# Kernel optimization log

Hardware: AMD Instinct MI355X
Metric: run time of the kernel (lower is better)

The kernel has to match this reference:

```python
import jax, jax.numpy as jnp
import numpy as np

N_MID = 100000
D = 64
B = 64
S = 256
K = 10
BIG_NEG = -2.0**32 + 1.0


def _din(q, facts, mask, W1, b1, W2, b2, W3, b3):
    # q broadcastable to facts shape; facts [..., T, D]; mask [..., T]
    qb = jnp.broadcast_to(q, facts.shape)
    x = jnp.concatenate([qb, facts, qb - facts, qb * facts], axis=-1)  # [..., T, 4D]
    h = jax.nn.sigmoid(x @ W1 + b1)
    h = jax.nn.sigmoid(h @ W2 + b2)
    s = (h @ W3 + b3)[..., 0]  # [..., T]
    s = jnp.where(mask == 1.0, s, BIG_NEG)
    a = jax.nn.softmax(s, axis=-1)
    return jnp.einsum('...t,...td->...d', a, facts)


def _prelu(x, alpha):
    return jnp.maximum(x, 0.0) + alpha * jnp.minimum(x, 0.0)


def setup_inputs():
    key = jax.random.key(0)
    ks = iter(jax.random.split(key, 48))
    def nrm(shape, scale=0.05):
        return jax.random.normal(next(ks), shape, dtype=jnp.float32) * scale
    inp = {}
    inp['mid'] = jax.random.randint(next(ks), (B,), 0, N_MID)
    inp['click_his'] = jax.random.randint(next(ks), (B, S), 0, N_MID)
    inp['unclick_his'] = jax.random.randint(next(ks), (B, K * S), 0, N_MID)
    inp['click_mask'] = jnp.ones((B, S), jnp.float32)
    inp['unclick_mask'] = jnp.ones((B, K * S), jnp.float32)
    inp['emb'] = nrm((N_MID, D), 0.1)
    for p in ('s', 'c', 'u'):  # search / click / unclick attention MLPs
        inp[p + 'W1'] = nrm((4 * D, 80)); inp[p + 'b1'] = jnp.zeros((80,), jnp.float32)
        inp[p + 'W2'] = nrm((80, 40));    inp[p + 'b2'] = jnp.zeros((40,), jnp.float32)
        inp[p + 'W3'] = nrm((40, 1));     inp[p + 'b3'] = jnp.zeros((1,), jnp.float32)
    F = 3 * D
    inp['bn_g'] = jnp.ones((F,), jnp.float32); inp['bn_b'] = jnp.zeros((F,), jnp.float32)
    inp['bn_m'] = jnp.zeros((F,), jnp.float32); inp['bn_v'] = jnp.ones((F,), jnp.float32)
    inp['fW1'] = nrm((F, 200)); inp['fb1'] = jnp.zeros((200,), jnp.float32); inp['a1'] = 0.25 * jnp.ones((200,), jnp.float32)
    inp['fW2'] = nrm((200, 80)); inp['fb2'] = jnp.zeros((80,), jnp.float32); inp['a2'] = 0.25 * jnp.ones((80,), jnp.float32)
    inp['fW3'] = nrm((80, 2)); inp['fb3'] = jnp.zeros((2,), jnp.float32)
    return inp


def reference(mid, click_his, unclick_his, click_mask, unclick_mask, emb,
              sW1, sb1, sW2, sb2, sW3, sb3,
              cW1, cb1, cW2, cb2, cW3, cb3,
              uW1, ub1, uW2, ub2, uW3, ub3,
              bn_g, bn_b, bn_m, bn_v,
              fW1, fb1, a1, fW2, fb2, a2, fW3, fb3):
    item = emb[mid]                                        # [B, D]
    click = emb[click_his] * click_mask[..., None]         # [B, S, D]
    unclick = emb[unclick_his] * unclick_mask[..., None]   # [B, K*S, D]
    uf = unclick.reshape(B, S, K, D)
    umask = unclick_mask.reshape(B, S, K)
    # din_attention_1: per clicked item, attend over its K unclicked items
    un_att = _din(click[:, :, None, :], uf, umask, sW1, sb1, sW2, sb2, sW3, sb3)  # [B, S, D]
    # denoise: project unclick rep onto click rep (shared component)
    dot = jnp.sum(un_att * click, axis=-1, keepdims=True)
    nrm2 = jnp.sum(click * click, axis=-1, keepdims=True) + 1e-12  # ||target||^2
    shared = dot * click / nrm2
    att1 = _din(item[:, None, :], click + shared, click_mask, cW1, cb1, cW2, cb2, cW3, cb3)  # [B, D]
    att2 = _din(item[:, None, :], un_att, click_mask, uW1, ub1, uW2, ub2, uW3, ub3)          # [B, D]
    x = jnp.concatenate([item, att1, att2], axis=-1)  # [B, 3D]
    x = (x - bn_m) / jnp.sqrt(bn_v + 1e-3) * bn_g + bn_b  # inference batchnorm
    x = _prelu(x @ fW1 + fb1, a1)
    x = _prelu(x @ fW2 + fb2, a2)
    logits = x @ fW3 + fb3
    return jax.nn.softmax(logits, axis=-1) + 1e-8
```

## Files before the change

### kernel.cpp

```cpp
#include <hip/hip_runtime.h>
#include <hip/hip_bf16.h>
#include <math.h>

#define BB 64
#define SS 256
#define KK 10
#define DD 64
#define FF 192
#define FH1 200
#define FH2 80
#define BIG_NEG_F (-4294967295.0f)

#define XSTR 200
#define H1STR 104
#define H2STR 49

#define W1ELTS (80 * XSTR)
#define W2ELTS (48 * H1STR)
#define WREG   (W1ELTS + W2ELTS)

typedef __bf16 bfrag __attribute__((ext_vector_type(8)));
typedef float f32x4 __attribute__((ext_vector_type(4)));

__device__ __forceinline__ float sigm_(float x) { return 1.0f / (1.0f + __expf(-x)); }

__global__ __launch_bounds__(256) void k_prep(
    const float* __restrict__ sW1, const float* __restrict__ sW2,
    const float* __restrict__ cW1, const float* __restrict__ cW2,
    const float* __restrict__ uW1, const float* __restrict__ uW2,
    __bf16* __restrict__ Wt)
{
    const int p = blockIdx.x;
    const float* W1 = (p == 0) ? sW1 : (p == 1) ? cW1 : uW1;
    const float* W2 = (p == 0) ? sW2 : (p == 1) ? cW2 : uW2;
    __bf16* o1 = Wt + p * WREG;
    __bf16* o2 = o1 + W1ELTS;
    for (int e = threadIdx.x; e < W1ELTS; e += 256) {
        const int n = e / XSTR, k = e % XSTR;
        float v = 0.0f;
        if (k < 64)       v = W1[k * 80 + n] + W1[(128 + k) * 80 + n];
        else if (k < 128) { const int kk = k - 64;  v = W1[(64 + kk) * 80 + n] - W1[(128 + kk) * 80 + n]; }
        else if (k < 192) { const int kk = k - 128; v = W1[(192 + kk) * 80 + n]; }
        o1[e] = (__bf16)v;
    }
    for (int e = threadIdx.x; e < W2ELTS; e += 256) {
        const int n = e / H1STR, k = e % H1STR;
        o2[e] = (__bf16)((n < 40 && k < 80) ? W2[k * 40 + n] : 0.0f);
    }
}

__global__ __launch_bounds__(320, 2) void k_din0(
    const int* __restrict__ click_his, const int* __restrict__ unclick_his,
    const float* __restrict__ click_mask, const float* __restrict__ unclick_mask,
    const float* __restrict__ emb, const __bf16* __restrict__ Wt,
    const float* __restrict__ b1, const float* __restrict__ b2,
    const float* __restrict__ W3, const float* __restrict__ b3,
    float* __restrict__ unatt, float* __restrict__ coef)
{
    __shared__ __align__(16) __bf16 sW1[80 * XSTR];
    __shared__ __align__(16) __bf16 sW2[48 * H1STR];
    __shared__ __align__(16) __bf16 sX [80 * XSTR];
    __shared__ float ssc[80];

    const int t = threadIdx.x;
    const int wave = t >> 6, lane = t & 63;
    const int quad = lane >> 4, l15 = lane & 15;
    const int r  = t >> 2;
    const int c0 = (t & 3) << 4;

    {
        const uint4* s1 = (const uint4*)(Wt);
        uint4* d1 = (uint4*)sW1;
        for (int e = t; e < W1ELTS / 8; e += 320) d1[e] = s1[e];
        const uint4* s2 = (const uint4*)(Wt + W1ELTS);
        uint4* d2 = (uint4*)sW2;
        for (int e = t; e < W2ELTS / 8; e += 320) d2[e] = s2[e];
    }

    float4 pq[4], pf[4];
    float pqs, pfs;
    auto loadrow = [&](int tl) {
        const int m  = tl * 80 + r;
        const int bs = tl * 8 + r / 10;
        const float* qp = emb + (size_t)click_his[bs] * DD;
        const float* fp = emb + (size_t)unclick_his[m] * DD;
        pqs = click_mask[bs];
        pfs = unclick_mask[m];
        #pragma unroll
        for (int i = 0; i < 4; ++i) {
            pq[i] = *(const float4*)(qp + c0 + 4 * i);
            pf[i] = *(const float4*)(fp + c0 + 4 * i);
        }
    };
    loadrow(blockIdx.x);

    for (int tile = blockIdx.x; tile < 2048; tile += 512) {
        {
            float qa[16], fa[16];
            #pragma unroll
            for (int i = 0; i < 4; ++i) {
                *(float4*)(qa + 4 * i) = pq[i];
                *(float4*)(fa + 4 * i) = pf[i];
            }
            __bf16* xr = sX + r * XSTR;
            #pragma unroll
            for (int h = 0; h < 2; ++h) {
                bfrag vq, vf, vm;
                #pragma unroll
                for (int j = 0; j < 8; ++j) {
                    const float qv = qa[h * 8 + j] * pqs;
                    const float fv = fa[h * 8 + j] * pfs;
                    vq[j] = (__bf16)qv; vf[j] = (__bf16)fv; vm[j] = (__bf16)(qv * fv);
                }
                *(bfrag*)(xr + c0 + h * 8)       = vq;
                *(bfrag*)(xr + 64 + c0 + h * 8)  = vf;
                *(bfrag*)(xr + 128 + c0 + h * 8) = vm;
            }
        }
        __syncthreads();

        if (tile + 512 < 2048) loadrow(tile + 512);

        bfrag af[6];
        {
            const __bf16* xrow = sX + (wave * 16 + l15) * XSTR + quad * 8;
            #pragma unroll
            for (int kc = 0; kc < 6; ++kc) af[kc] = *(const bfrag*)(xrow + kc * 32);
        }
        f32x4 acc[5];
        #pragma unroll
        for (int nt = 0; nt < 5; ++nt) acc[nt] = (f32x4){0.f, 0.f, 0.f, 0.f};
        {
            const __bf16* wbase = sW1 + l15 * XSTR + quad * 8;
            #pragma unroll
            for (int nt = 0; nt < 5; ++nt) {
                const __bf16* wp = wbase + nt * 16 * XSTR;
                #pragma unroll
                for (int kc = 0; kc < 6; ++kc)
                    acc[nt] = __builtin_amdgcn_mfma_f32_16x16x32_bf16(
                        af[kc], *(const bfrag*)(wp + kc * 32), acc[nt], 0, 0, 0);
            }
        }
        __syncthreads();

        __bf16* sH1 = sX;
        #pragma unroll
        for (int nt = 0; nt < 5; ++nt) {
            const int n = nt * 16 + l15;
            const float bb = b1[n];
            #pragma unroll
            for (int rg = 0; rg < 4; ++rg) {
                const int row = wave * 16 + quad * 4 + rg;
                sH1[row * H1STR + n] = (__bf16)sigm_(acc[nt][rg] + bb);
            }
        }
        for (int e = t; e < 80 * 16; e += 320) {
            const int row = e >> 4, cc = 80 + (e & 15);
            sH1[row * H1STR + cc] = (__bf16)0.0f;
        }
        __syncthreads();

        bfrag af2[3];
        {
            const __bf16* hrow = sH1 + (wave * 16 + l15) * H1STR + quad * 8;
            #pragma unroll
            for (int kc = 0; kc < 3; ++kc) af2[kc] = *(const bfrag*)(hrow + kc * 32);
        }
        f32x4 acc2[3];
        #pragma unroll
        for (int nt = 0; nt < 3; ++nt) acc2[nt] = (f32x4){0.f, 0.f, 0.f, 0.f};
        {
            const __bf16* wbase = sW2 + l15 * H1STR + quad * 8;
            #pragma unroll
            for (int nt = 0; nt < 3; ++nt) {
                const __bf16* wp = wbase + nt * 16 * H1STR;
                #pragma unroll
                for (int kc = 0; kc < 3; ++kc)
                    acc2[nt] = __builtin_amdgcn_mfma_f32_16x16x32_bf16(
                        af2[kc], *(const bfrag*)(wp + kc * 32), acc2[nt], 0, 0, 0);
            }
        }
        __syncthreads();

        float* sH2 = (float*)sX;
        #pragma unroll
        for (int nt = 0; nt < 3; ++nt) {
            const int n = nt * 16 + l15;
            if (n < 40) {
                const float bb = b2[n];
                #pragma unroll
                for (int rg = 0; rg < 4; ++rg) {
                    const int row = wave * 16 + quad * 4 + rg;
                    sH2[row * H2STR + n] = sigm_(acc2[nt][rg] + bb);
                }
            }
        }
        __syncthreads();

        if (t < 80) {
            float s = b3[0];
            #pragma unroll 8
            for (int i = 0; i < 40; ++i) s += sH2[t * H2STR + i] * W3[i];
            const int m = tile * 80 + t;
            ssc[t] = (unclick_mask[m] == 1.0f) ? s : BIG_NEG_F;
        }
        __syncthreads();

        for (int j = wave; j < 8; j += 5) {
            const int bs = tile * 8 + j;
            float a[KK];
            float mx = -INFINITY;
            #pragma unroll
            for (int k = 0; k < KK; ++k) { a[k] = ssc[j * KK + k]; mx = fmaxf(mx, a[k]); }
            float sum = 0.0f;
            #pragma unroll
            for (int k = 0; k < KK; ++k) { a[k] = __expf(a[k] - mx); sum += a[k]; }
            const float inv = 1.0f / sum;
            float acc3 = 0.0f;
            #pragma unroll
            for (int k = 0; k < KK; ++k) {
                const int off = bs * KK + k;
                acc3 += a[k] * (emb[(size_t)unclick_his[off] * DD + lane] * unclick_mask[off]);
            }
            acc3 *= inv;
            unatt[bs * DD + lane] = acc3;
            const float qv = emb[(size_t)click_his[bs] * DD + lane] * click_mask[bs];
            float dp = acc3 * qv, nq = qv * qv;
            #pragma unroll
            for (int o = 32; o > 0; o >>= 1) {
                dp += __shfl_down(dp, o, 64);
                nq += __shfl_down(nq, o, 64);
            }
            if (lane == 0) coef[bs] = 1.0f + dp / (nq + 1e-12f);
        }
        __syncthreads();
    }
}

__global__ __launch_bounds__(256, 2) void k_din12(
    const int* __restrict__ mid, const int* __restrict__ click_his,
    const float* __restrict__ click_mask,
    const float* __restrict__ emb, const float* __restrict__ unatt,
    const float* __restrict__ coef, const __bf16* __restrict__ Wt,
    const float* __restrict__ cb1, const float* __restrict__ cb2,
    const float* __restrict__ cW3, const float* __restrict__ cb3,
    const float* __restrict__ ub1, const float* __restrict__ ub2,
    const float* __restrict__ uW3, const float* __restrict__ ub3,
    float* __restrict__ scores_c, float* __restrict__ scores_u)
{
    __shared__ __align__(16) __bf16 sW1[80 * XSTR];
    __shared__ __align__(16) __bf16 sW2[48 * H1STR];
    __shared__ __align__(16) __bf16 sX [64 * XSTR];

    const int t = threadIdx.x;
    const int mode = blockIdx.y;
    const int wave = t >> 6, lane = t & 63;
    const int quad = lane >> 4, l15 = lane & 15;

    const float* b1 = mode ? ub1 : cb1;
    const float* b2 = mode ? ub2 : cb2;
    const float* W3 = mode ? uW3 : cW3;
    const float* b3 = mode ? ub3 : cb3;
    const __bf16* wreg = Wt + (mode + 1) * WREG;

    {
        const uint4* s1 = (const uint4*)(wreg);
        uint4* d1 = (uint4*)sW1;
        for (int e = t; e < W1ELTS / 8; e += 256) d1[e] = s1[e];
        const uint4* s2 = (const uint4*)(wreg + W1ELTS);
        uint4* d2 = (uint4*)sW2;
        for (int e = t; e < W2ELTS / 8; e += 256) d2[e] = s2[e];
    }

    {
        const int r  = t >> 2;
        const int c0 = (t & 3) << 4;
        const int m  = blockIdx.x * 64 + r;
        const int b  = m >> 8;
        const float* qp = emb + (size_t)mid[b] * DD;
        const float* fp; float fs;
        if (mode == 0) { fp = emb + (size_t)click_his[m] * DD; fs = click_mask[m] * coef[m]; }
        else           { fp = unatt + (size_t)m * DD; fs = 1.0f; }
        float qa[16], fa[16];
        #pragma unroll
        for (int i = 0; i < 4; ++i) {
            *(float4*)(qa + 4 * i) = *(const float4*)(qp + c0 + 4 * i);
            *(float4*)(fa + 4 * i) = *(const float4*)(fp + c0 + 4 * i);
        }
        __bf16* xr = sX + r * XSTR;
        #pragma unroll
        for (int h = 0; h < 2; ++h) {
            bfrag vq, vf, vm;
            #pragma unroll
            for (int j = 0; j < 8; ++j) {
                const float qv = qa[h * 8 + j];
                const float fv = fa[h * 8 + j] * fs;
                vq[j] = (__bf16)qv; vf[j] = (__bf16)fv; vm[j] = (__bf16)(qv * fv);
            }
            *(bfrag*)(xr + c0 + h * 8)       = vq;
            *(bfrag*)(xr + 64 + c0 + h * 8)  = vf;
            *(bfrag*)(xr + 128 + c0 + h * 8) = vm;
        }
    }
    __syncthreads();

    bfrag af[6];
    {
        const __bf16* xrow = sX + (wave * 16 + l15) * XSTR + quad * 8;
        #pragma unroll
        for (int kc = 0; kc < 6; ++kc) af[kc] = *(const bfrag*)(xrow + kc * 32);
    }
    f32x4 acc[5];
    #pragma unroll
    for (int nt = 0; nt < 5; ++nt) acc[nt] = (f32x4){0.f, 0.f, 0.f, 0.f};
    {
        const __bf16* wbase = sW1 + l15 * XSTR + quad * 8;
        #pragma unroll
        for (int nt = 0; nt < 5; ++nt) {
            const __bf16* wp = wbase + nt * 16 * XSTR;
            #pragma unroll
            for (int kc = 0; kc < 6; ++kc)
                acc[nt] = __builtin_amdgcn_mfma_f32_16x16x32_bf16(
                    af[kc], *(const bfrag*)(wp + kc * 32), acc[nt], 0, 0, 0);
        }
    }
    __syncthreads();

    __bf16* sH1 = sX;
    #pragma unroll
    for (int nt = 0; nt < 5; ++nt) {
        const int n = nt * 16 + l15;
        const float bb = b1[n];
        #pragma unroll
        for (int rg = 0; rg < 4; ++rg) {
            const int row = wave * 16 + quad * 4 + rg;
            sH1[row * H1STR + n] = (__bf16)sigm_(acc[nt][rg] + bb);
        }
    }
    for (int e = t; e < 64 * 16; e += 256) {
        const int row = e >> 4, cc = 80 + (e & 15);
        sH1[row * H1STR + cc] = (__bf16)0.0f;
    }
    __syncthreads();

    bfrag af2[3];
    {
        const __bf16* hrow = sH1 + (wave * 16 + l15) * H1STR + quad * 8;
        #pragma unroll
        for (int kc = 0; kc < 3; ++kc) af2[kc] = *(const bfrag*)(hrow + kc * 32);
    }
    f32x4 acc2[3];
    #pragma unroll
    for (int nt = 0; nt < 3; ++nt) acc2[nt] = (f32x4){0.f, 0.f, 0.f, 0.f};
    {
        const __bf16* wbase = sW2 + l15 * H1STR + quad * 8;
        #pragma unroll
        for (int nt = 0; nt < 3; ++nt) {
            const __bf16* wp = wbase + nt * 16 * H1STR;
            #pragma unroll
            for (int kc = 0; kc < 3; ++kc)
                acc2[nt] = __builtin_amdgcn_mfma_f32_16x16x32_bf16(
                    af2[kc], *(const bfrag*)(wp + kc * 32), acc2[nt], 0, 0, 0);
        }
    }
    __syncthreads();

    float* sH2 = (float*)sX;
    #pragma unroll
    for (int nt = 0; nt < 3; ++nt) {
        const int n = nt * 16 + l15;
        if (n < 40) {
            const float bb = b2[n];
            #pragma unroll
            for (int rg = 0; rg < 4; ++rg) {
                const int row = wave * 16 + quad * 4 + rg;
                sH2[row * H2STR + n] = sigm_(acc2[nt][rg] + bb);
            }
        }
    }
    __syncthreads();

    if (t < 64) {
        float s = b3[0];
        #pragma unroll 8
        for (int i = 0; i < 40; ++i) s += sH2[t * H2STR + i] * W3[i];
        const int m = blockIdx.x * 64 + t;
        const float sc = (click_mask[m] == 1.0f) ? s : BIG_NEG_F;
        (mode ? scores_u : scores_c)[m] = sc;
    }
}

__global__ __launch_bounds__(256) void k_tail(
    const int* __restrict__ mid, const int* __restrict__ click_his,
    const float* __restrict__ click_mask,
    const float* __restrict__ emb, const float* __restrict__ unatt,
    const float* __restrict__ coef,
    const float* __restrict__ scores_c, const float* __restrict__ scores_u,
    const float* __restrict__ bn_g, const float* __restrict__ bn_b,
    const float* __restrict__ bn_m, const float* __restrict__ bn_v,
    const float* __restrict__ fW1, const float* __restrict__ fb1, const float* __restrict__ a1,
    const float* __restrict__ fW2, const float* __restrict__ fb2, const float* __restrict__ a2,
    const float* __restrict__ fW3, const float* __restrict__ fb3,
    float* __restrict__ out)
{
    const int b = blockIdx.x, t = threadIdx.x;
    const int lane = t & 63, wv = t >> 6;

    __shared__ float x[FF];
    __shared__ float sa[SS];
    __shared__ float red[8];
    __shared__ float part[4][DD];
    __shared__ float h1[FH1];
    __shared__ float h2[FH2];

    if (t < DD) x[t] = emb[(size_t)mid[b] * DD + t];

    for (int ty = 0; ty < 2; ++ty) {
        const float sc = (ty ? scores_u : scores_c)[b * SS + t];
        float m = sc;
        #pragma unroll
        for (int o = 32; o > 0; o >>= 1) m = fmaxf(m, __shfl_down(m, o, 64));
        if (lane == 0) red[wv] = m;
        __syncthreads();
        m = fmaxf(fmaxf(red[0], red[1]), fmaxf(red[2], red[3]));
        const float e = __expf(sc - m);
        sa[t] = e;
        float s = e;
        #pragma unroll
        for (int o = 32; o > 0; o >>= 1) s += __shfl_down(s, o, 64);
        if (lane == 0) red[4 + wv] = s;
        __syncthreads();
        const float inv = 1.0f / (red[4] + red[5] + red[6] + red[7]);

        float acc = 0.0f;
        for (int s2 = wv * 64; s2 < wv * 64 + 64; ++s2) {
            const int bs = b * SS + s2;
            const float fv = ty ? unatt[(size_t)bs * DD + lane]
                                : emb[(size_t)click_his[bs] * DD + lane] * click_mask[bs] * coef[bs];
            acc += sa[s2] * inv * fv;
        }
        part[wv][lane] = acc;
        __syncthreads();
        if (t < DD) x[DD + ty * DD + t] = part[0][t] + part[1][t] + part[2][t] + part[3][t];
        __syncthreads();
    }

    if (t < FF) x[t] = (x[t] - bn_m[t]) * rsqrtf(bn_v[t] + 1e-3f) * bn_g[t] + bn_b[t];
    __syncthreads();
    if (t < FH1) {
        float acc = fb1[t];
        #pragma unroll 4
        for (int i = 0; i < FF; ++i) acc += x[i] * fW1[i * FH1 + t];
        h1[t] = fmaxf(acc, 0.0f) + a1[t] * fminf(acc, 0.0f);
    }
    __syncthreads();
    if (t < FH2) {
        float acc = fb2[t];
        #pragma unroll 4
        for (int i = 0; i < FH1; ++i) acc += h1[i] * fW2[i * FH2 + t];
        h2[t] = fmaxf(acc, 0.0f) + a2[t] * fminf(acc, 0.0f);
    }
    __syncthreads();
    if (t == 0) {
        float l0 = fb3[0], l1 = fb3[1];
        for (int i = 0; i < FH2; ++i) {
            l0 += h2[i] * fW3[i * 2 + 0];
            l1 += h2[i] * fW3[i * 2 + 1];
        }
        const float mx = fmaxf(l0, l1);
        const float e0 = __expf(l0 - mx), e1 = __expf(l1 - mx);
        const float inv = 1.0f / (e0 + e1);
        out[b * 2 + 0] = e0 * inv + 1e-8f;
        out[b * 2 + 1] = e1 * inv + 1e-8f;
    }
}

extern "C" void kernel_launch(void* const* d_in, const int* in_sizes, int n_in,
                              void* d_out, int out_size, void* d_ws, size_t ws_size,
                              hipStream_t stream) {
    const int*   mid          = (const int*)d_in[0];
    const int*   click_his    = (const int*)d_in[1];
    const int*   unclick_his  = (const int*)d_in[2];
    const float* click_mask   = (const float*)d_in[3];
    const float* unclick_mask = (const float*)d_in[4];
    const float* emb          = (const float*)d_in[5];
    const float* sW1 = (const float*)d_in[6];  const float* sb1 = (const float*)d_in[7];
    const float* sW2 = (const float*)d_in[8];  const float* sb2 = (const float*)d_in[9];
    const float* sW3 = (const float*)d_in[10]; const float* sb3 = (const float*)d_in[11];
    const float* cW1 = (const float*)d_in[12]; const float* cb1 = (const float*)d_in[13];
    const float* cW2 = (const float*)d_in[14]; const float* cb2 = (const float*)d_in[15];
    const float* cW3 = (const float*)d_in[16]; const float* cb3 = (const float*)d_in[17];
    const float* uW1 = (const float*)d_in[18]; const float* ub1 = (const float*)d_in[19];
    const float* uW2 = (const float*)d_in[20]; const float* ub2 = (const float*)d_in[21];
    const float* uW3 = (const float*)d_in[22]; const float* ub3 = (const float*)d_in[23];
    const float* bn_g = (const float*)d_in[24]; const float* bn_b = (const float*)d_in[25];
    const float* bn_m = (const float*)d_in[26]; const float* bn_v = (const float*)d_in[27];
    const float* fW1 = (const float*)d_in[28]; const float* fb1 = (const float*)d_in[29];
    const float* a1  = (const float*)d_in[30];
    const float* fW2 = (const float*)d_in[31]; const float* fb2 = (const float*)d_in[32];
    const float* a2  = (const float*)d_in[33];
    const float* fW3 = (const float*)d_in[34]; const float* fb3 = (const float*)d_in[35];

    float* out = (float*)d_out;

    char* w = (char*)d_ws;
    __bf16* Wt      = (__bf16*)(w + 0);
    float* scores_c = (float*)(w + 125952);
    float* scores_u = (float*)(w + 191488);
    float* coef     = (float*)(w + 257024);
    float* unatt    = (float*)(w + 322560);

    hipLaunchKernelGGL(k_prep, dim3(3), dim3(256), 0, stream,
        sW1, sW2, cW1, cW2, uW1, uW2, Wt);

    hipLaunchKernelGGL(k_din0, dim3(512), dim3(320), 0, stream,
        click_his, unclick_his, click_mask, unclick_mask, emb, Wt,
        sb1, sb2, sW3, sb3, unatt, coef);

    hipLaunchKernelGGL(k_din12, dim3(256, 2), dim3(256), 0, stream,
        mid, click_his, click_mask, emb, unatt, coef, Wt,
        cb1, cb2, cW3, cb3, ub1, ub2, uW3, ub3, scores_c, scores_u);

    hipLaunchKernelGGL(k_tail, dim3(BB), dim3(256), 0, stream,
        mid, click_his, click_mask, emb, unatt, coef, scores_c, scores_u,
        bn_g, bn_b, bn_m, bn_v, fW1, fb1, a1, fW2, fb2, a2, fW3, fb3, out);
}
```

Measured before the change: 271.3 us.

## Build MFMA operands in registers, keep W2 in registers, launch one tile per block

Both attention kernels now build the layer-1 MFMA A-fragments straight from the gathered embeddings in registers instead of staging them in shared memory. Layer-2 weights now live in registers, and the layer-3 dot product is done with a wave-level shuffle reduction, which removes most __syncthreads barriers and the sH2/sW2 shared buffers. k_din0 drops its persistent loop with register prefetch and launches 2048 blocks, one tile each, and the weight-prep kernel is spread over 30 blocks. This cuts LDS traffic and barriers and raises occupancy, but each block now reloads the W1 weights into shared memory and there is no cross-tile prefetch.

```diff
diff --git a/kernel.cpp b/kernel.cpp
--- a/kernel.cpp
+++ b/kernel.cpp
@@ -13,7 +13,6 @@
 
 #define XSTR 200
 #define H1STR 104
-#define H2STR 49
 
 #define W1ELTS (80 * XSTR)
 #define W2ELTS (48 * H1STR)
@@ -30,12 +29,12 @@
     const float* __restrict__ uW1, const float* __restrict__ uW2,
     __bf16* __restrict__ Wt)
 {
-    const int p = blockIdx.x;
+    const int p = blockIdx.x, g = blockIdx.y;
     const float* W1 = (p == 0) ? sW1 : (p == 1) ? cW1 : uW1;
     const float* W2 = (p == 0) ? sW2 : (p == 1) ? cW2 : uW2;
     __bf16* o1 = Wt + p * WREG;
     __bf16* o2 = o1 + W1ELTS;
-    for (int e = threadIdx.x; e < W1ELTS; e += 256) {
+    for (int e = g * 256 + threadIdx.x; e < W1ELTS; e += 2560) {
         const int n = e / XSTR, k = e % XSTR;
         float v = 0.0f;
         if (k < 64)       v = W1[k * 80 + n] + W1[(128 + k) * 80 + n];
@@ -43,13 +42,89 @@
         else if (k < 192) { const int kk = k - 128; v = W1[(192 + kk) * 80 + n]; }
         o1[e] = (__bf16)v;
     }
-    for (int e = threadIdx.x; e < W2ELTS; e += 256) {
+    for (int e = g * 256 + threadIdx.x; e < W2ELTS; e += 2560) {
         const int n = e / H1STR, k = e % H1STR;
         o2[e] = (__bf16)((n < 40 && k < 80) ? W2[k * 40 + n] : 0.0f);
     }
 }
 
-__global__ __launch_bounds__(320, 2) void k_din0(
+__device__ __forceinline__ void mlp_core(
+    const float* qv, const float* fv,
+    const __bf16* __restrict__ sW1, __bf16* __restrict__ sH1w,
+    const bfrag* wb2, const float* b1v, const float* b2v, const float* w3v,
+    int quad, int l15, float* score)
+{
+    bfrag af[6];
+    #pragma unroll
+    for (int j = 0; j < 8; ++j) {
+        af[0][j] = (__bf16)qv[j];
+        af[1][j] = (__bf16)qv[8 + j];
+        af[2][j] = (__bf16)fv[j];
+        af[3][j] = (__bf16)fv[8 + j];
+        af[4][j] = (__bf16)(qv[j] * fv[j]);
+        af[5][j] = (__bf16)(qv[8 + j] * fv[8 + j]);
+    }
+
+    f32x4 acc[5];
+    #pragma unroll
+    for (int nt = 0; nt < 5; ++nt) acc[nt] = (f32x4){0.f, 0.f, 0.f, 0.f};
+    {
+        const __bf16* wbase = sW1 + l15 * XSTR + quad * 8;
+        #pragma unroll
+        for (int nt = 0; nt < 5; ++nt) {
+            const __bf16* wp = wbase + nt * 16 * XSTR;
+            #pragma unroll
+            for (int kc = 0; kc < 6; ++kc)
+                acc[nt] = __builtin_amdgcn_mfma_f32_16x16x32_bf16(
+                    af[kc], *(const bfrag*)(wp + kc * 32), acc[nt], 0, 0, 0);
+        }
+    }
+
+    #pragma unroll
+    for (int nt = 0; nt < 5; ++nt) {
+        #pragma unroll
+        for (int rg = 0; rg < 4; ++rg)
+            sH1w[(quad * 4 + rg) * H1STR + nt * 16 + l15] =
+                (__bf16)sigm_(acc[nt][rg] + b1v[nt]);
+    }
+    #pragma unroll
+    for (int rg = 0; rg < 4; ++rg)
+        sH1w[(quad * 4 + rg) * H1STR + 80 + l15] = (__bf16)0.0f;
+
+    bfrag af2[3];
+    {
+        const __bf16* hrow = sH1w + l15 * H1STR + quad * 8;
+        #pragma unroll
+        for (int kc = 0; kc < 3; ++kc) af2[kc] = *(const bfrag*)(hrow + kc * 32);
+    }
+    f32x4 acc2[3];
+    #pragma unroll
+    for (int nt = 0; nt < 3; ++nt) acc2[nt] = (f32x4){0.f, 0.f, 0.f, 0.f};
+    #pragma unroll
+    for (int nt = 0; nt < 3; ++nt)
+        #pragma unroll
+        for (int kc = 0; kc < 3; ++kc)
+            acc2[nt] = __builtin_amdgcn_mfma_f32_16x16x32_bf16(
+                af2[kc], wb2[nt * 3 + kc], acc2[nt], 0, 0, 0);
+
+    float part[4] = {0.f, 0.f, 0.f, 0.f};
+    #pragma unroll
+    for (int nt = 0; nt < 3; ++nt) {
+        #pragma unroll
+        for (int rg = 0; rg < 4; ++rg)
+            part[rg] += sigm_(acc2[nt][rg] + b2v[nt]) * w3v[nt];
+    }
+    #pragma unroll
+    for (int off = 1; off < 16; off <<= 1) {
+        #pragma unroll
+        for (int rg = 0; rg < 4; ++rg)
+            part[rg] += __shfl_xor(part[rg], off, 64);
+    }
+    #pragma unroll
+    for (int rg = 0; rg < 4; ++rg) score[rg] = part[rg];
+}
+
+__global__ __launch_bounds__(320) void k_din0(
     const int* __restrict__ click_his, const int* __restrict__ unclick_his,
     const float* __restrict__ click_mask, const float* __restrict__ unclick_mask,
     const float* __restrict__ emb, const __bf16* __restrict__ Wt,
@@ -58,186 +133,104 @@
     float* __restrict__ unatt, float* __restrict__ coef)
 {
     __shared__ __align__(16) __bf16 sW1[80 * XSTR];
-    __shared__ __align__(16) __bf16 sW2[48 * H1STR];
-    __shared__ __align__(16) __bf16 sX [80 * XSTR];
+    __shared__ __align__(16) __bf16 sH1[5 * 16 * H1STR];
     __shared__ float ssc[80];
 
     const int t = threadIdx.x;
     const int wave = t >> 6, lane = t & 63;
     const int quad = lane >> 4, l15 = lane & 15;
-    const int r  = t >> 2;
-    const int c0 = (t & 3) << 4;
-
-    {
-        const uint4* s1 = (const uint4*)(Wt);
+
+    {
+        const uint4* s1 = (const uint4*)Wt;
         uint4* d1 = (uint4*)sW1;
         for (int e = t; e < W1ELTS / 8; e += 320) d1[e] = s1[e];
-        const uint4* s2 = (const uint4*)(Wt + W1ELTS);
-        uint4* d2 = (uint4*)sW2;
-        for (int e = t; e < W2ELTS / 8; e += 320) d2[e] = s2[e];
-    }
-
-    float4 pq[4], pf[4];
-    float pqs, pfs;
-    auto loadrow = [&](int tl) {
-        const int m  = tl * 80 + r;
-        const int bs = tl * 8 + r / 10;
+    }
+
+    bfrag wb2[9];
+    float b1v[5], b2v[3], w3v[3];
+    {
+        const __bf16* w2g = Wt + W1ELTS;
+        #pragma unroll
+        for (int nt = 0; nt < 3; ++nt)
+            #pragma unroll
+            for (int kc = 0; kc < 3; ++kc)
+                wb2[nt * 3 + kc] = *(const bfrag*)(w2g + (nt * 16 + l15) * H1STR + kc * 32 + quad * 8);
+        #pragma unroll
+        for (int nt = 0; nt < 5; ++nt) b1v[nt] = b1[nt * 16 + l15];
+        #pragma unroll
+        for (int nt = 0; nt < 3; ++nt) {
+            const int n = nt * 16 + l15;
+            b2v[nt] = (n < 40) ? b2[n] : 0.0f;
+            w3v[nt] = (n < 40) ? W3[n] : 0.0f;
+        }
+    }
+    const float b3v = b3[0];
+
+    const int row = 16 * wave + l15;
+    const int m   = blockIdx.x * 80 + row;
+    const int bs  = blockIdx.x * 8 + row / 10;
+    float qv[16], fv[16];
+    {
         const float* qp = emb + (size_t)click_his[bs] * DD;
         const float* fp = emb + (size_t)unclick_his[m] * DD;
-        pqs = click_mask[bs];
-        pfs = unclick_mask[m];
-        #pragma unroll
-        for (int i = 0; i < 4; ++i) {
-            pq[i] = *(const float4*)(qp + c0 + 4 * i);
-            pf[i] = *(const float4*)(fp + c0 + 4 * i);
-        }
-    };
-    loadrow(blockIdx.x);
-
-    for (int tile = blockIdx.x; tile < 2048; tile += 512) {
-        {
-            float qa[16], fa[16];
-            #pragma unroll
-            for (int i = 0; i < 4; ++i) {
-                *(float4*)(qa + 4 * i) = pq[i];
-                *(float4*)(fa + 4 * i) = pf[i];
-            }
-            __bf16* xr = sX + r * XSTR;
-            #pragma unroll
-            for (int h = 0; h < 2; ++h) {
-                bfrag vq, vf, vm;
-                #pragma unroll
-                for (int j = 0; j < 8; ++j) {
-                    const float qv = qa[h * 8 + j] * pqs;
-                    const float fv = fa[h * 8 + j] * pfs;
-                    vq[j] = (__bf16)qv; vf[j] = (__bf16)fv; vm[j] = (__bf16)(qv * fv);
-                }
-                *(bfrag*)(xr + c0 + h * 8)       = vq;
-                *(bfrag*)(xr + 64 + c0 + h * 8)  = vf;
-                *(bfrag*)(xr + 128 + c0 + h * 8) = vm;
-            }
-        }
-        __syncthreads();
-
-        if (tile + 512 < 2048) loadrow(tile + 512);
-
-        bfrag af[6];
-        {
-            const __bf16* xrow = sX + (wave * 16 + l15) * XSTR + quad * 8;
-            #pragma unroll
-            for (int kc = 0; kc < 6; ++kc) af[kc] = *(const bfrag*)(xrow + kc * 32);
-        }
-        f32x4 acc[5];
-        #pragma unroll
-        for (int nt = 0; nt < 5; ++nt) acc[nt] = (f32x4){0.f, 0.f, 0.f, 0.f};
-        {
-            const __bf16* wbase = sW1 + l15 * XSTR + quad * 8;
-            #pragma unroll
-            for (int nt = 0; nt < 5; ++nt) {
-                const __bf16* wp = wbase + nt * 16 * XSTR;
-                #pragma unroll
-                for (int kc = 0; kc < 6; ++kc)
-                    acc[nt] = __builtin_amdgcn_mfma_f32_16x16x32_bf16(
-                        af[kc], *(const bfrag*)(wp + kc * 32), acc[nt], 0, 0, 0);
-            }
-        }
-        __syncthreads();
-
-        __bf16* sH1 = sX;
-        #pragma unroll
-        for (int nt = 0; nt < 5; ++nt) {
-            const int n = nt * 16 + l15;
-            const float bb = b1[n];
-            #pragma unroll
-            for (int rg = 0; rg < 4; ++rg) {
-                const int row = wave * 16 + quad * 4 + rg;
-                sH1[row * H1STR + n] = (__bf16)sigm_(acc[nt][rg] + bb);
-            }
-        }
-        for (int e = t; e < 80 * 16; e += 320) {
-            const int row = e >> 4, cc = 80 + (e & 15);
-            sH1[row * H1STR + cc] = (__bf16)0.0f;
-        }
-        __syncthreads();
-
-        bfrag af2[3];
-        {
-            const __bf16* hrow = sH1 + (wave * 16 + l15) * H1STR + quad * 8;
-            #pragma unroll
-            for (int kc = 0; kc < 3; ++kc) af2[kc] = *(const bfrag*)(hrow + kc * 32);
-        }
-        f32x4 acc2[3];
-        #pragma unroll
-        for (int nt = 0; nt < 3; ++nt) acc2[nt] = (f32x4){0.f, 0.f, 0.f, 0.f};
-        {
-            const __bf16* wbase = sW2 + l15 * H1STR + quad * 8;
-            #pragma unroll
-            for (int nt = 0; nt < 3; ++nt) {
-                const __bf16* wp = wbase + nt * 16 * H1STR;
-                #pragma unroll
-                for (int kc = 0; kc < 3; ++kc)
-                    acc2[nt] = __builtin_amdgcn_mfma_f32_16x16x32_bf16(
-                        af2[kc], *(const bfrag*)(wp + kc * 32), acc2[nt], 0, 0, 0);
-            }
-        }
-        __syncthreads();
-
-        float* sH2 = (float*)sX;
-        #pragma unroll
-        for (int nt = 0; nt < 3; ++nt) {
-            const int n = nt * 16 + l15;
-            if (n < 40) {
-                const float bb = b2[n];
-                #pragma unroll
-                for (int rg = 0; rg < 4; ++rg) {
-                    const int row = wave * 16 + quad * 4 + rg;
-                    sH2[row * H2STR + n] = sigm_(acc2[nt][rg] + bb);
-                }
-            }
-        }
-        __syncthreads();
-
-        if (t < 80) {
-            float s = b3[0];
-            #pragma unroll 8
-            for (int i = 0; i < 40; ++i) s += sH2[t * H2STR + i] * W3[i];
-            const int m = tile * 80 + t;
-            ssc[t] = (unclick_mask[m] == 1.0f) ? s : BIG_NEG_F;
-        }
-        __syncthreads();
-
-        for (int j = wave; j < 8; j += 5) {
-            const int bs = tile * 8 + j;
-            float a[KK];
-            float mx = -INFINITY;
-            #pragma unroll
-            for (int k = 0; k < KK; ++k) { a[k] = ssc[j * KK + k]; mx = fmaxf(mx, a[k]); }
-            float sum = 0.0f;
-            #pragma unroll
-            for (int k = 0; k < KK; ++k) { a[k] = __expf(a[k] - mx); sum += a[k]; }
-            const float inv = 1.0f / sum;
-            float acc3 = 0.0f;
-            #pragma unroll
-            for (int k = 0; k < KK; ++k) {
-                const int off = bs * KK + k;
-                acc3 += a[k] * (emb[(size_t)unclick_his[off] * DD + lane] * unclick_mask[off]);
-            }
-            acc3 *= inv;
-            unatt[bs * DD + lane] = acc3;
-            const float qv = emb[(size_t)click_his[bs] * DD + lane] * click_mask[bs];
-            float dp = acc3 * qv, nq = qv * qv;
-            #pragma unroll
-            for (int o = 32; o > 0; o >>= 1) {
-                dp += __shfl_down(dp, o, 64);
-                nq += __shfl_down(nq, o, 64);
-            }
-            if (lane == 0) coef[bs] = 1.0f + dp / (nq + 1e-12f);
-        }
-        __syncthreads();
-    }
-}
-
-__global__ __launch_bounds__(256, 2) void k_din12(
+        const float qs = click_mask[bs], fs = unclick_mask[m];
+        const int c = quad * 8;
+        *(float4*)(qv + 0)  = *(const float4*)(qp + c);
+        *(float4*)(qv + 4)  = *(const float4*)(qp + c + 4);
+        *(float4*)(qv + 8)  = *(const float4*)(qp + 32 + c);
+        *(float4*)(qv + 12) = *(const float4*)(qp + 32 + c + 4);
+        *(float4*)(fv + 0)  = *(const float4*)(fp + c);
+        *(float4*)(fv + 4)  = *(const float4*)(fp + c + 4);
+        *(float4*)(fv + 8)  = *(const float4*)(fp + 32 + c);
+        *(float4*)(fv + 12) = *(const float4*)(fp + 32 + c + 4);
+        #pragma unroll
+        for (int i = 0; i < 16; ++i) { qv[i] *= qs; fv[i] *= fs; }
+    }
+    __syncthreads();
+
+    float score[4];
+    mlp_core(qv, fv, sW1, sH1 + wave * 16 * H1STR, wb2, b1v, b2v, w3v, quad, l15, score);
+
+    if (l15 == 0) {
+        #pragma unroll
+        for (int rg = 0; rg < 4; ++rg) {
+            const int r2 = 16 * wave + quad * 4 + rg;
+            const int m2 = blockIdx.x * 80 + r2;
+            ssc[r2] = (unclick_mask[m2] == 1.0f) ? (score[rg] + b3v) : BIG_NEG_F;
+        }
+    }
+    __syncthreads();
+
+    for (int j = wave; j < 8; j += 5) {
+        const int bsj = blockIdx.x * 8 + j;
+        float a[KK];
+        float mx = -INFINITY;
+        #pragma unroll
+        for (int k = 0; k < KK; ++k) { a[k] = ssc[j * KK + k]; mx = fmaxf(mx, a[k]); }
+        float sum = 0.0f;
+        #pragma unroll
+        for (int k = 0; k < KK; ++k) { a[k] = __expf(a[k] - mx); sum += a[k]; }
+        const float inv = 1.0f / sum;
+        float acc3 = 0.0f;
+        #pragma unroll
+        for (int k = 0; k < KK; ++k) {
+            const int off = bsj * KK + k;
+            acc3 += a[k] * (emb[(size_t)unclick_his[off] * DD + lane] * unclick_mask[off]);
+        }
+        acc3 *= inv;
+        unatt[(size_t)bsj * DD + lane] = acc3;
+        const float qv2 = emb[(size_t)click_his[bsj] * DD + lane] * click_mask[bsj];
+        float dp = acc3 * qv2, nq = qv2 * qv2;
+        #pragma unroll
+        for (int o = 32; o > 0; o >>= 1) {
+            dp += __shfl_down(dp, o, 64);
+            nq += __shfl_down(nq, o, 64);
+        }
+        if (lane == 0) coef[bsj] = 1.0f + dp / (nq + 1e-12f);
+    }
+}
+
+__global__ __launch_bounds__(256) void k_din12(
     const int* __restrict__ mid, const int* __restrict__ click_his,
     const float* __restrict__ click_mask,
     const float* __restrict__ emb, const float* __restrict__ unatt,
@@ -249,8 +242,7 @@
     float* __restrict__ scores_c, float* __restrict__ scores_u)
 {
     __shared__ __align__(16) __bf16 sW1[80 * XSTR];
-    __shared__ __align__(16) __bf16 sW2[48 * H1STR];
-    __shared__ __align__(16) __bf16 sX [64 * XSTR];
+    __shared__ __align__(16) __bf16 sH1[4 * 16 * H1STR];
 
     const int t = threadIdx.x;
     const int mode = blockIdx.y;
@@ -264,129 +256,64 @@
     const __bf16* wreg = Wt + (mode + 1) * WREG;
 
     {
-        const uint4* s1 = (const uint4*)(wreg);
+        const uint4* s1 = (const uint4*)wreg;
         uint4* d1 = (uint4*)sW1;
         for (int e = t; e < W1ELTS / 8; e += 256) d1[e] = s1[e];
-        const uint4* s2 = (const uint4*)(wreg + W1ELTS);
-        uint4* d2 = (uint4*)sW2;
-        for (int e = t; e < W2ELTS / 8; e += 256) d2[e] = s2[e];
-    }
-
-    {
-        const int r  = t >> 2;
-        const int c0 = (t & 3) << 4;
-        const int m  = blockIdx.x * 64 + r;
-        const int b  = m >> 8;
+    }
+
+    bfrag wb2[9];
+    float b1v[5], b2v[3], w3v[3];
+    {
+        const __bf16* w2g = wreg + W1ELTS;
+        #pragma unroll
+        for (int nt = 0; nt < 3; ++nt)
+            #pragma unroll
+            for (int kc = 0; kc < 3; ++kc)
+                wb2[nt * 3 + kc] = *(const bfrag*)(w2g + (nt * 16 + l15) * H1STR + kc * 32 + quad * 8);
+        #pragma unroll
+        for (int nt = 0; nt < 5; ++nt) b1v[nt] = b1[nt * 16 + l15];
+        #pragma unroll
+        for (int nt = 0; nt < 3; ++nt) {
+            const int n = nt * 16 + l15;
+            b2v[nt] = (n < 40) ? b2[n] : 0.0f;
+            w3v[nt] = (n < 40) ? W3[n] : 0.0f;
+        }
+    }
+    const float b3v = b3[0];
+
+    const int row = 16 * wave + l15;
+    const int m   = blockIdx.x * 64 + row;
+    const int b   = m >> 8;
+    float qv[16], fv[16];
+    {
         const float* qp = emb + (size_t)mid[b] * DD;
         const float* fp; float fs;
         if (mode == 0) { fp = emb + (size_t)click_his[m] * DD; fs = click_mask[m] * coef[m]; }
         else           { fp = unatt + (size_t)m * DD; fs = 1.0f; }
-        float qa[16], fa[16];
-        #pragma unroll
-        for (int i = 0; i < 4; ++i) {
-            *(float4*)(qa + 4 * i) = *(const float4*)(qp + c0 + 4 * i);
-            *(float4*)(fa + 4 * i) = *(const float4*)(fp + c0 + 4 * i);
-        }
-        __bf16* xr = sX + r * XSTR;
-        #pragma unroll
-        for (int h = 0; h < 2; ++h) {
-            bfrag vq, vf, vm;
-            #pragma unroll
-            for (int j = 0; j < 8; ++j) {
-                const float qv = qa[h * 8 + j];
-                const float fv = fa[h * 8 + j] * fs;
-                vq[j] = (__bf16)qv; vf[j] = (__bf16)fv; vm[j] = (__bf16)(qv * fv);
-            }
-            *(bfrag*)(xr + c0 + h * 8)       = vq;
-            *(bfrag*)(xr + 64 + c0 + h * 8)  = vf;
-            *(bfrag*)(xr + 128 + c0 + h * 8) = vm;
-        }
-    }
-    __syncthreads();
-
-    bfrag af[6];
-    {
-        const __bf16* xrow = sX + (wave * 16 + l15) * XSTR + quad * 8;
-        #pragma unroll
-        for (int kc = 0; kc < 6; ++kc) af[kc] = *(const bfrag*)(xrow + kc * 32);
-    }
-    f32x4 acc[5];
-    #pragma unroll
-    for (int nt = 0; nt < 5; ++nt) acc[nt] = (f32x4){0.f, 0.f, 0.f, 0.f};
-    {
-        const __bf16* wbase = sW1 + l15 * XSTR + quad * 8;
-        #pragma unroll
-        for (int nt = 0; nt < 5; ++nt) {
-            const __bf16* wp = wbase + nt * 16 * XSTR;
-            #pragma unroll
-            for (int kc = 0; kc < 6; ++kc)
-                acc[nt] = __builtin_amdgcn_mfma_f32_16x16x32_bf16(
-                    af[kc], *(const bfrag*)(wp + kc * 32), acc[nt], 0, 0, 0);
-        }
-    }
-    __syncthreads();
-
-    __bf16* sH1 = sX;
-    #pragma unroll
-    for (int nt = 0; nt < 5; ++nt) {
-        const int n = nt * 16 + l15;
-        const float bb = b1[n];
+        const int c = quad * 8;
+        *(float4*)(qv + 0)  = *(const float4*)(qp + c);
+        *(float4*)(qv + 4)  = *(const float4*)(qp + c + 4);
+        *(float4*)(qv + 8)  = *(const float4*)(qp + 32 + c);
+        *(float4*)(qv + 12) = *(const float4*)(qp + 32 + c + 4);
+        *(float4*)(fv + 0)  = *(const float4*)(fp + c);
+        *(float4*)(fv + 4)  = *(const float4*)(fp + c + 4);
+        *(float4*)(fv + 8)  = *(const float4*)(fp + 32 + c);
+        *(float4*)(fv + 12) = *(const float4*)(fp + 32 + c + 4);
+        #pragma unroll
+        for (int i = 0; i < 16; ++i) fv[i] *= fs;
+    }
+    __syncthreads();
+
+    float score[4];
+    mlp_core(qv, fv, sW1, sH1 + wave * 16 * H1STR, wb2, b1v, b2v, w3v, quad, l15, score);
+
+    if (l15 == 0) {
+        float* dst = mode ? scores_u : scores_c;
         #pragma unroll
         for (int rg = 0; rg < 4; ++rg) {
-            const int row = wave * 16 + quad * 4 + rg;
-            sH1[row * H1STR + n] = (__bf16)sigm_(acc[nt][rg] + bb);
-        }
-    }
-    for (int e = t; e < 64 * 16; e += 256) {
-        const int row = e >> 4, cc = 80 + (e & 15);
-        sH1[row * H1STR + cc] = (__bf16)0.0f;
-    }
-    __syncthreads();
-
-    bfrag af2[3];
-    {
-        const __bf16* hrow = sH1 + (wave * 16 + l15) * H1STR + quad * 8;
-        #pragma unroll
-        for (int kc = 0; kc < 3; ++kc) af2[kc] = *(const bfrag*)(hrow + kc * 32);
-    }
-    f32x4 acc2[3];
-    #pragma unroll
-    for (int nt = 0; nt < 3; ++nt) acc2[nt] = (f32x4){0.f, 0.f, 0.f, 0.f};
-    {
-        const __bf16* wbase = sW2 + l15 * H1STR + quad * 8;
-        #pragma unroll
-        for (int nt = 0; nt < 3; ++nt) {
-            const __bf16* wp = wbase + nt * 16 * H1STR;
-            #pragma unroll
-            for (int kc = 0; kc < 3; ++kc)
-                acc2[nt] = __builtin_amdgcn_mfma_f32_16x16x32_bf16(
-                    af2[kc], *(const bfrag*)(wp + kc * 32), acc2[nt], 0, 0, 0);
-        }
-    }
-    __syncthreads();
-
-    float* sH2 = (float*)sX;
-    #pragma unroll
-    for (int nt = 0; nt < 3; ++nt) {
-        const int n = nt * 16 + l15;
-        if (n < 40) {
-            const float bb = b2[n];
-            #pragma unroll
-            for (int rg = 0; rg < 4; ++rg) {
-                const int row = wave * 16 + quad * 4 + rg;
-                sH2[row * H2STR + n] = sigm_(acc2[nt][rg] + bb);
-            }
-        }
-    }
-    __syncthreads();
-
-    if (t < 64) {
-        float s = b3[0];
-        #pragma unroll 8
-        for (int i = 0; i < 40; ++i) s += sH2[t * H2STR + i] * W3[i];
-        const int m = blockIdx.x * 64 + t;
-        const float sc = (click_mask[m] == 1.0f) ? s : BIG_NEG_F;
-        (mode ? scores_u : scores_c)[m] = sc;
+            const int m2 = blockIdx.x * 64 + 16 * wave + quad * 4 + rg;
+            dst[m2] = (click_mask[m2] == 1.0f) ? (score[rg] + b3v) : BIG_NEG_F;
+        }
     }
 }
 
@@ -435,9 +362,9 @@
         float acc = 0.0f;
         for (int s2 = wv * 64; s2 < wv * 64 + 64; ++s2) {
             const int bs = b * SS + s2;
-            const float fv = ty ? unatt[(size_t)bs * DD + lane]
-                                : emb[(size_t)click_his[bs] * DD + lane] * click_mask[bs] * coef[bs];
-            acc += sa[s2] * inv * fv;
+            const float fvv = ty ? unatt[(size_t)bs * DD + lane]
+                                 : emb[(size_t)click_his[bs] * DD + lane] * click_mask[bs] * coef[bs];
+            acc += sa[s2] * inv * fvv;
         }
         part[wv][lane] = acc;
         __syncthreads();
@@ -510,10 +437,10 @@
     float* coef     = (float*)(w + 257024);
     float* unatt    = (float*)(w + 322560);
 
-    hipLaunchKernelGGL(k_prep, dim3(3), dim3(256), 0, stream,
+    hipLaunchKernelGGL(k_prep, dim3(3, 10), dim3(256), 0, stream,
         sW1, sW2, cW1, cW2, uW1, uW2, Wt);
 
-    hipLaunchKernelGGL(k_din0, dim3(512), dim3(320), 0, stream,
+    hipLaunchKernelGGL(k_din0, dim3(2048), dim3(320), 0, stream,
         click_his, unclick_his, click_mask, unclick_mask, emb, Wt,
         sb1, sb2, sW3, sb3, unatt, coef);
 
```

After: 235.6 us. 1.15x faster.
